# Performance work log

Measured on AMD Instinct MI355X. Metric: run time of the kernel, lower is better.

Reference implementation:

```python
import jax, jax.numpy as jnp
import numpy as np

B, N, H = 8, 2048, 1024
FF = 4 * H
EPS = 1e-5

def layer_norm(x, g, b):
    mu = jnp.mean(x, axis=-1, keepdims=True)
    var = jnp.mean(jnp.square(x - mu), axis=-1, keepdims=True)
    return (x - mu) * jax.lax.rsqrt(var + EPS) * g + b

def setup_inputs() -> dict:
    key = jax.random.key(0)
    ks = jax.random.split(key, 6)
    s1 = 1.0 / np.sqrt(H)
    s2 = 1.0 / np.sqrt(FF)
    return {
        "x": jax.random.normal(ks[0], (B, N, H), dtype=jnp.float32),
        "ln1_g": jnp.ones((H,), jnp.float32),
        "ln1_b": jnp.zeros((H,), jnp.float32),
        "ln2_g": jnp.ones((H,), jnp.float32),
        "ln2_b": jnp.zeros((H,), jnp.float32),
        "w1": jax.random.uniform(ks[1], (H, FF), jnp.float32, -s1, s1),
        "b1": jax.random.uniform(ks[2], (FF,), jnp.float32, -s1, s1),
        "w2": jax.random.uniform(ks[3], (FF, H), jnp.float32, -s2, s2),
        "b2": jax.random.uniform(ks[4], (H,), jnp.float32, -s2, s2),
    }

def reference(x, ln1_g, ln1_b, ln2_g, ln2_b, w1, b1, w2, b2):
    # raw unscaled self-attention: softmax(x x^T) x  (dropout = identity, eval mode)
    scores = jnp.einsum('bnh,bmh->bnm', x, x)          # [B,N,N]
    attn = jax.nn.softmax(scores, axis=-1)
    attended = jnp.einsum('bnm,bmh->bnh', attn, x)     # [B,N,H]
    h = layer_norm(x + attended, ln1_g, ln1_b)
    ffn = jnp.einsum('bnf,fh->bnh', jax.nn.gelu(jnp.einsum('bnh,hf->bnf', h, w1) + b1, approximate=False), w2) + b2
    return layer_norm(h + ffn, ln2_g, ln2_b)
```

## Files before the change

### kernel.cpp

```cpp
#include <hip/hip_runtime.h>
#include <stdint.h>

#define NB 8
#define NN 2048
#define HH 1024
#define FFD 4096
#define M2 8
constexpr float EPS_ = 1e-5f;

typedef _Float16 f16;
typedef _Float16 f16x8 __attribute__((ext_vector_type(8)));
typedef float f32x4 __attribute__((ext_vector_type(4)));
typedef float f32x16 __attribute__((ext_vector_type(16)));

__device__ __forceinline__ f32x4 MFMA16(f16x8 a, f16x8 b, f32x4 c) {
  return __builtin_amdgcn_mfma_f32_16x16x32_f16(a, b, c, 0, 0, 0);
}
__device__ __forceinline__ f32x16 MFMA32(f16x8 a, f16x8 b, f32x16 c) {
  return __builtin_amdgcn_mfma_f32_32x32x16_f16(a, b, c, 0, 0, 0);
}
__device__ __forceinline__ ushort h2u(f16 h) { union { f16 h; ushort u; } v; v.h = h; return v.u; }
__device__ __forceinline__ unsigned pack2(float a, float b) {
  return (unsigned)h2u((f16)a) | ((unsigned)h2u((f16)b) << 16);
}
__device__ __forceinline__ float4 ld4(const float* p) { return *(const float4*)p; }
__device__ __forceinline__ float gelu(float u) {
  return 0.5f * u * (1.0f + erff(u * 0.70710678118654752f));
}
__device__ __forceinline__ void gload16(const void* g, void* l) {
  __builtin_amdgcn_global_load_lds(
      (const __attribute__((address_space(1))) unsigned int*)g,
      (__attribute__((address_space(3))) unsigned int*)l, 16, 0, 0);
}

__global__ void convert_hl(const float* __restrict__ x, f16* __restrict__ xh,
                           f16* __restrict__ xl) {
  const size_t i = ((size_t)blockIdx.x * blockDim.x + threadIdx.x) * 4;
  float4 v = ld4(x + i);
  f16 h0 = (f16)v.x, h1 = (f16)v.y, h2 = (f16)v.z, h3 = (f16)v.w;
  ushort4 ho = {h2u(h0), h2u(h1), h2u(h2), h2u(h3)};
  ushort4 lo = {h2u((f16)(v.x - (float)h0)), h2u((f16)(v.y - (float)h1)),
                h2u((f16)(v.z - (float)h2)), h2u((f16)(v.w - (float)h3))};
  *(ushort4*)(xh + i) = ho;
  *(ushort4*)(xl + i) = lo;
}

__global__ void transpose_f16k(const float* __restrict__ src, f16* __restrict__ dst,
                               int R, int C, long sbs, long dbs) {
  __shared__ float tl[32][33];
  src += (size_t)blockIdx.z * sbs;
  dst += (size_t)blockIdx.z * dbs;
  const int t = threadIdx.x;
  const int c0 = blockIdx.x * 32, r0 = blockIdx.y * 32;
  {
    const int r = t >> 3, c4 = t & 7;
    float4 v = ld4(src + (size_t)(r0 + r) * C + c0 + c4 * 4);
    tl[r][c4 * 4 + 0] = v.x; tl[r][c4 * 4 + 1] = v.y;
    tl[r][c4 * 4 + 2] = v.z; tl[r][c4 * 4 + 3] = v.w;
  }
  __syncthreads();
  {
    const int c = t >> 3, r4 = t & 7;
    ushort4 o;
    o.x = h2u((f16)tl[r4 * 4 + 0][c]);
    o.y = h2u((f16)tl[r4 * 4 + 1][c]);
    o.z = h2u((f16)tl[r4 * 4 + 2][c]);
    o.w = h2u((f16)tl[r4 * 4 + 3][c]);
    *(ushort4*)(dst + (size_t)(c0 + c) * R + r0 + r4 * 4) = o;
  }
}

#define RSTR 528
__device__ __forceinline__ void stageKB(char* REGb, const f16* xhb, const f16* xlb,
                                        int j0, int k0, int w, int l) {
#pragma unroll
  for (int r = 0; r < 2; ++r) {
    const int grp = r * 8 + w;
    const int j = grp * 16 + (l >> 2);
    const int clog = (l & 3) ^ ((j >> 1) & 3);
    const size_t src = (size_t)(j0 + j) * HH + k0 + clog * 8;
    gload16(xhb + src, REGb + grp * 1024);
    gload16(xlb + src, REGb + 16384 + grp * 1024);
  }
}
__device__ __forceinline__ void stageVB(char* VBb, const f16* xtb, int jabs, int w, int l) {
#pragma unroll
  for (int r = 0; r < 4; ++r) {
    const int grp = r * 8 + w;
    const int h = grp * 32 + (l >> 1);
    const int clog = (l & 1) ^ ((h >> 2) & 1);
    gload16(xtb + (size_t)h * NN + jabs + clog * 8, VBb + grp * 1024);
  }
}

__global__ __launch_bounds__(512, 2)
void attn_v2(const float* __restrict__ x, const f16* __restrict__ xh,
             const f16* __restrict__ xl, const f16* __restrict__ xt,
             const float* __restrict__ g1, const float* __restrict__ lb1,
             float* __restrict__ hout) {
  extern __shared__ char smem[];
  char* REG = smem;
  char* PB  = smem + 65536;
  float* RD   = (float*)(smem + 99328);
  float* mrow = (float*)(smem + 100352);
  float* lrow = (float*)(smem + 100608);
  float* fctb = (float*)(smem + 100864);

  const int t = threadIdx.x, l = t & 63, w = t >> 6;
  const int l31 = l & 31, lh = l >> 5;
  const int wr = w >> 2, wc = w & 3;
  const int b = blockIdx.y, m0 = blockIdx.x * 64;
  const f16* __restrict__ xhb = xh + (size_t)b * NN * HH;
  const f16* __restrict__ xlb = xl + (size_t)b * NN * HH;
  const f16* __restrict__ xtb = xt + (size_t)b * HH * NN;
  const float* __restrict__ xb = x + (size_t)b * NN * HH;

  if (t < 64) { mrow[t] = -INFINITY; lrow[t] = 0.f; }

  f32x16 Oacc[8] = {};
  const int arow = m0 + wr * 32 + l31;

  for (int jt = 0; jt < 8; ++jt) {
    const int j0 = jt * 256;
    f32x16 sacc[2] = {};

    f16x8 ah[2], al[2];
#pragma unroll
    for (int s = 0; s < 2; ++s) {
      ah[s] = *(const f16x8*)(xhb + (size_t)arow * HH + s * 16 + lh * 8);
      al[s] = *(const f16x8*)(xlb + (size_t)arow * HH + s * 16 + lh * 8);
    }
    stageKB(REG, xhb, xlb, j0, 0, w, l);
    __syncthreads();
    int buf = 0;
    for (int kc = 0; kc < 32; ++kc) {
      f16x8 nh[2], nl[2];
      if (kc < 31) {
        stageKB(REG + (buf ^ 1) * 32768, xhb, xlb, j0, (kc + 1) * 32, w, l);
        const int kn = (kc + 1) * 32;
#pragma unroll
        for (int s = 0; s < 2; ++s) {
          nh[s] = *(const f16x8*)(xhb + (size_t)arow * HH + kn + s * 16 + lh * 8);
          nl[s] = *(const f16x8*)(xlb + (size_t)arow * HH + kn + s * 16 + lh * 8);
        }
      }
      const char* KH = REG + buf * 32768;
      const char* KL = KH + 16384;
#pragma unroll
      for (int ct = 0; ct < 2; ++ct) {
        const int j = wc * 64 + ct * 32 + l31;
        const int swz = (j >> 1) & 3;
        const char* rowH = KH + j * 64;
        const char* rowL = KL + j * 64;
#pragma unroll
        for (int s = 0; s < 2; ++s) {
          const int cp = (s * 2 + lh) ^ swz;
          f16x8 bh = *(const f16x8*)(rowH + cp * 16);
          f16x8 bl = *(const f16x8*)(rowL + cp * 16);
          sacc[ct] = MFMA32(ah[s], bh, sacc[ct]);
          sacc[ct] = MFMA32(al[s], bh, sacc[ct]);
          sacc[ct] = MFMA32(ah[s], bl, sacc[ct]);
        }
      }
      __syncthreads();
      if (kc < 31) {
#pragma unroll
        for (int s = 0; s < 2; ++s) { ah[s] = nh[s]; al[s] = nl[s]; }
      }
      buf ^= 1;
    }

    float tmax[16];
#pragma unroll
    for (int rg = 0; rg < 16; ++rg) tmax[rg] = fmaxf(sacc[0][rg], sacc[1][rg]);
#pragma unroll
    for (int off = 1; off <= 16; off <<= 1)
#pragma unroll
      for (int rg = 0; rg < 16; ++rg) tmax[rg] = fmaxf(tmax[rg], __shfl_xor(tmax[rg], off, 64));
    if (l31 == 0) {
#pragma unroll
      for (int rg = 0; rg < 16; ++rg) {
        const int rl = (rg & 3) + 8 * (rg >> 2) + 4 * lh;
        RD[wc * 64 + wr * 32 + rl] = tmax[rg];
      }
    }
    __syncthreads();
    if (t < 64) {
      float mt = fmaxf(fmaxf(RD[t], RD[64 + t]), fmaxf(RD[128 + t], RD[192 + t]));
      float mo = mrow[t];
      float mn = fmaxf(mo, mt);
      mrow[t] = mn;
      fctb[t] = __expf(mo - mn);
    }
    __syncthreads();
    float mv[16], psum[16];
#pragma unroll
    for (int rg = 0; rg < 16; ++rg)
      mv[rg] = mrow[wr * 32 + (rg & 3) + 8 * (rg >> 2) + 4 * lh];
#pragma unroll
    for (int ct = 0; ct < 2; ++ct) {
#pragma unroll
      for (int rg = 0; rg < 16; ++rg) {
        float p = __expf(sacc[ct][rg] - mv[rg]);
        if (ct == 0) psum[rg] = p; else psum[rg] += p;
        float po = __shfl_xor(p, 1, 64);
        if (!(l & 1)) {
          const int R = wr * 32 + (rg & 3) + 8 * (rg >> 2) + 4 * lh;
          const int col = wc * 64 + ct * 32 + l31;
          *(unsigned*)(PB + R * RSTR + col * 2) = pack2(p, po);
        }
      }
    }
#pragma unroll
    for (int off = 1; off <= 16; off <<= 1)
#pragma unroll
      for (int rg = 0; rg < 16; ++rg) psum[rg] += __shfl_xor(psum[rg], off, 64);
    if (l31 == 0) {
#pragma unroll
      for (int rg = 0; rg < 16; ++rg) {
        const int rl = (rg & 3) + 8 * (rg >> 2) + 4 * lh;
        RD[wc * 64 + wr * 32 + rl] = psum[rg];
      }
    }
    __syncthreads();
    if (t < 64) lrow[t] = lrow[t] * fctb[t] + (RD[t] + RD[64 + t] + RD[128 + t] + RD[192 + t]);
    float fv[16];
#pragma unroll
    for (int rg = 0; rg < 16; ++rg)
      fv[rg] = fctb[wr * 32 + (rg & 3) + 8 * (rg >> 2) + 4 * lh];
#pragma unroll
    for (int ht = 0; ht < 8; ++ht)
#pragma unroll
      for (int rg = 0; rg < 16; ++rg) Oacc[ht][rg] *= fv[rg];

    stageVB(REG, xtb, j0, w, l);
    __syncthreads();
    int vbuf = 0;
    for (int jc = 0; jc < 16; ++jc) {
      if (jc < 15) stageVB(REG + (vbuf ^ 1) * 32768, xtb, j0 + (jc + 1) * 16, w, l);
      const char* VBc = REG + vbuf * 32768;
      f16x8 pa = *(const f16x8*)(PB + (wr * 32 + l31) * RSTR + (jc * 2 + lh) * 16);
#pragma unroll
      for (int ht = 0; ht < 8; ++ht) {
        const int h = wc * 256 + ht * 32 + l31;
        f16x8 vb = *(const f16x8*)(VBc + h * 32 + ((lh ^ ((h >> 2) & 1)) * 16));
        Oacc[ht] = MFMA32(pa, vb, Oacc[ht]);
      }
      __syncthreads();
      vbuf ^= 1;
    }
  }

  float lv[16];
#pragma unroll
  for (int rg = 0; rg < 16; ++rg)
    lv[rg] = 1.0f / lrow[wr * 32 + (rg & 3) + 8 * (rg >> 2) + 4 * lh];
  float musum[16];
#pragma unroll
  for (int rg = 0; rg < 16; ++rg) musum[rg] = 0.f;
#pragma unroll
  for (int ht = 0; ht < 8; ++ht) {
    const int col = wc * 256 + ht * 32 + l31;
#pragma unroll
    for (int rg = 0; rg < 16; ++rg) {
      const int R = wr * 32 + (rg & 3) + 8 * (rg >> 2) + 4 * lh;
      float v = fmaf(Oacc[ht][rg], lv[rg], xb[(size_t)(m0 + R) * HH + col]);
      Oacc[ht][rg] = v; musum[rg] += v;
    }
  }
#pragma unroll
  for (int off = 1; off <= 16; off <<= 1)
#pragma unroll
    for (int rg = 0; rg < 16; ++rg) musum[rg] += __shfl_xor(musum[rg], off, 64);
  if (l31 == 0) {
#pragma unroll
    for (int rg = 0; rg < 16; ++rg) {
      const int rl = (rg & 3) + 8 * (rg >> 2) + 4 * lh;
      RD[wc * 64 + wr * 32 + rl] = musum[rg];
    }
  }
  __syncthreads();
  if (t < 64) mrow[t] = (RD[t] + RD[64 + t] + RD[128 + t] + RD[192 + t]) * (1.0f / HH);
  __syncthreads();
  float mu[16], vsum[16];
#pragma unroll
  for (int rg = 0; rg < 16; ++rg) {
    mu[rg] = mrow[wr * 32 + (rg & 3) + 8 * (rg >> 2) + 4 * lh];
    vsum[rg] = 0.f;
  }
#pragma unroll
  for (int ht = 0; ht < 8; ++ht)
#pragma unroll
    for (int rg = 0; rg < 16; ++rg) {
      float d = Oacc[ht][rg] - mu[rg];
      vsum[rg] += d * d;
    }
#pragma unroll
  for (int off = 1; off <= 16; off <<= 1)
#pragma unroll
    for (int rg = 0; rg < 16; ++rg) vsum[rg] += __shfl_xor(vsum[rg], off, 64);
  if (l31 == 0) {
#pragma unroll
    for (int rg = 0; rg < 16; ++rg) {
      const int rl = (rg & 3) + 8 * (rg >> 2) + 4 * lh;
      RD[wc * 64 + wr * 32 + rl] = vsum[rg];
    }
  }
  __syncthreads();
  if (t < 64) fctb[t] = rsqrtf((RD[t] + RD[64 + t] + RD[128 + t] + RD[192 + t]) * (1.0f / HH) + EPS_);
  __syncthreads();
  float rs[16];
#pragma unroll
  for (int rg = 0; rg < 16; ++rg)
    rs[rg] = fctb[wr * 32 + (rg & 3) + 8 * (rg >> 2) + 4 * lh];
#pragma unroll
  for (int ht = 0; ht < 8; ++ht) {
    const int col = wc * 256 + ht * 32 + l31;
    const float gv = g1[col], bv = lb1[col];
#pragma unroll
    for (int rg = 0; rg < 16; ++rg) {
      const int R = wr * 32 + (rg & 3) + 8 * (rg >> 2) + 4 * lh;
      hout[((size_t)b * NN + m0 + R) * HH + col] = (Oacc[ht][rg] - mu[rg]) * rs[rg] * gv + bv;
    }
  }
}

__global__ __launch_bounds__(1024)
void attn_legacy(const float* __restrict__ x, const float* __restrict__ g1,
                 const float* __restrict__ lb1, float* __restrict__ hout) {
  extern __shared__ char smem[];
  char* AB = smem;
  char* BB = smem + 5120;
  char* PB2 = smem + 46080;
  char* VB = smem + 62976;
  float* RD  = (float*)(smem + 144896);
  float* RD2 = (float*)(smem + 145920);

  const int t = threadIdx.x, l = t & 63, w = t >> 6;
  const int lg = l >> 4, li = l & 15;
  const int wr = w >> 3, wc = w & 7;
  const int b = blockIdx.y, m0 = blockIdx.x * 32;
  const float* __restrict__ xb = x + (size_t)b * NN * HH;

  const int ar = t >> 5, ak = t & 31;
  const int bj = t >> 2, bq = t & 3;
  const int vjp = t & 15, vhg = t >> 4;

  f32x4 Oacc[8] = {};
  float m_run[4] = {-INFINITY, -INFINITY, -INFINITY, -INFINITY};
  float l_run[4] = {0.f, 0.f, 0.f, 0.f};

  for (int jt = 0; jt < 8; ++jt) {
    const int j0 = jt * 256;
    f32x4 sacc[2] = {};
    float qv = xb[(size_t)(m0 + ar) * HH + ak];
    float4 ca = ld4(xb + (size_t)(j0 + bj) * HH + bq * 8);
    float4 cb = ld4(xb + (size_t)(j0 + bj) * HH + bq * 8 + 4);
    for (int kc = 0; kc < 32; ++kc) {
      __syncthreads();
      {
        f16 qh = (f16)qv; f16 ql = (f16)(qv - (float)qh);
        *(ushort*)(AB + ar * 80 + ak * 2) = h2u(qh);
        *(ushort*)(AB + 2560 + ar * 80 + ak * 2) = h2u(ql);
        float vv[8] = {ca.x, ca.y, ca.z, ca.w, cb.x, cb.y, cb.z, cb.w};
        f16x8 hi8, lo8;
#pragma unroll
        for (int i = 0; i < 8; ++i) {
          f16 h = (f16)vv[i]; hi8[i] = h; lo8[i] = (f16)(vv[i] - (float)h);
        }
        *(f16x8*)(BB + bj * 80 + bq * 16) = hi8;
        *(f16x8*)(BB + 20480 + bj * 80 + bq * 16) = lo8;
      }
      if (kc < 31) {
        const int k0 = (kc + 1) * 32;
        qv = xb[(size_t)(m0 + ar) * HH + k0 + ak];
        ca = ld4(xb + (size_t)(j0 + bj) * HH + k0 + bq * 8);
        cb = ld4(xb + (size_t)(j0 + bj) * HH + k0 + bq * 8 + 4);
      }
      __syncthreads();
      const int arow = wr * 16 + li;
      f16x8 ahi = *(const f16x8*)(AB + arow * 80 + lg * 16);
      f16x8 alo = *(const f16x8*)(AB + 2560 + arow * 80 + lg * 16);
#pragma unroll
      for (int ct = 0; ct < 2; ++ct) {
        const int j = wc * 32 + ct * 16 + li;
        f16x8 bhi = *(const f16x8*)(BB + j * 80 + lg * 16);
        f16x8 blo = *(const f16x8*)(BB + 20480 + j * 80 + lg * 16);
        sacc[ct] = MFMA16(ahi, bhi, sacc[ct]);
        sacc[ct] = MFMA16(ahi, blo, sacc[ct]);
        sacc[ct] = MFMA16(alo, bhi, sacc[ct]);
      }
    }
    float m[4];
#pragma unroll
    for (int r = 0; r < 4; ++r) m[r] = fmaxf(sacc[0][r], sacc[1][r]);
#pragma unroll
    for (int off = 1; off <= 8; off <<= 1)
#pragma unroll
      for (int r = 0; r < 4; ++r) m[r] = fmaxf(m[r], __shfl_xor(m[r], off, 64));
    if (li == 0)
#pragma unroll
      for (int r = 0; r < 4; ++r) RD[wc * 32 + wr * 16 + lg * 4 + r] = m[r];
    __syncthreads();
    float mnew[4], fct[4];
#pragma unroll
    for (int r = 0; r < 4; ++r) {
      const int row = wr * 16 + lg * 4 + r;
      float mt = RD[row];
#pragma unroll
      for (int w2 = 1; w2 < 8; ++w2) mt = fmaxf(mt, RD[w2 * 32 + row]);
      mnew[r] = fmaxf(m_run[r], mt);
      fct[r] = __expf(m_run[r] - mnew[r]);
      m_run[r] = mnew[r];
    }
    float psum[4] = {0.f, 0.f, 0.f, 0.f};
#pragma unroll
    for (int ct = 0; ct < 2; ++ct)
#pragma unroll
      for (int r = 0; r < 4; ++r) {
        float p = __expf(sacc[ct][r] - mnew[r]);
        psum[r] += p;
        float po = __shfl_xor(p, 1, 64);
        if (!(l & 1)) {
          const int row = wr * 16 + lg * 4 + r;
          *(unsigned*)(PB2 + row * 528 + (wc * 32 + ct * 16 + (li & 14)) * 2) = pack2(p, po);
        }
      }
#pragma unroll
    for (int off = 1; off <= 8; off <<= 1)
#pragma unroll
      for (int r = 0; r < 4; ++r) psum[r] += __shfl_xor(psum[r], off, 64);
    if (li == 0)
#pragma unroll
      for (int r = 0; r < 4; ++r) RD2[wc * 32 + wr * 16 + lg * 4 + r] = psum[r];
    __syncthreads();
#pragma unroll
    for (int r = 0; r < 4; ++r) {
      const int row = wr * 16 + lg * 4 + r;
      float ts = 0.f;
#pragma unroll
      for (int w2 = 0; w2 < 8; ++w2) ts += RD2[w2 * 32 + row];
      l_run[r] = l_run[r] * fct[r] + ts;
    }
#pragma unroll
    for (int ti = 0; ti < 8; ++ti)
#pragma unroll
      for (int r = 0; r < 4; ++r) Oacc[ti][r] *= fct[r];

    float4 v0[4], v1[4];
#pragma unroll
    for (int q = 0; q < 4; ++q) {
      v0[q] = ld4(xb + (size_t)(j0 + 2 * vjp) * HH + vhg * 16 + q * 4);
      v1[q] = ld4(xb + (size_t)(j0 + 2 * vjp + 1) * HH + vhg * 16 + q * 4);
    }
    for (int jc = 0; jc < 8; ++jc) {
      __syncthreads();
#pragma unroll
      for (int q = 0; q < 4; ++q) {
        float a0[4] = {v0[q].x, v0[q].y, v0[q].z, v0[q].w};
        float a1[4] = {v1[q].x, v1[q].y, v1[q].z, v1[q].w};
#pragma unroll
        for (int i = 0; i < 4; ++i) {
          const int h = vhg * 16 + q * 4 + i;
          *(unsigned*)(VB + h * 80 + vjp * 4) = pack2(a0[i], a1[i]);
        }
      }
      if (jc < 7) {
        const int jj = j0 + (jc + 1) * 32;
#pragma unroll
        for (int q = 0; q < 4; ++q) {
          v0[q] = ld4(xb + (size_t)(jj + 2 * vjp) * HH + vhg * 16 + q * 4);
          v1[q] = ld4(xb + (size_t)(jj + 2 * vjp + 1) * HH + vhg * 16 + q * 4);
        }
      }
      __syncthreads();
      f16x8 pa = *(const f16x8*)(PB2 + (wr * 16 + li) * 528 + jc * 64 + lg * 16);
#pragma unroll
      for (int ti = 0; ti < 8; ++ti) {
        const int h = wc * 128 + ti * 16 + li;
        f16x8 vb = *(const f16x8*)(VB + h * 80 + lg * 16);
        Oacc[ti] = MFMA16(pa, vb, Oacc[ti]);
      }
    }
  }

  float musum[4] = {0.f, 0.f, 0.f, 0.f};
#pragma unroll
  for (int ti = 0; ti < 8; ++ti) {
    const int col = wc * 128 + ti * 16 + li;
#pragma unroll
    for (int r = 0; r < 4; ++r) {
      const int row = m0 + wr * 16 + lg * 4 + r;
      float v = xb[(size_t)row * HH + col] + Oacc[ti][r] / l_run[r];
      Oacc[ti][r] = v; musum[r] += v;
    }
  }
#pragma unroll
  for (int off = 1; off <= 8; off <<= 1)
#pragma unroll
    for (int r = 0; r < 4; ++r) musum[r] += __shfl_xor(musum[r], off, 64);
  if (li == 0)
#pragma unroll
    for (int r = 0; r < 4; ++r) RD[wc * 32 + wr * 16 + lg * 4 + r] = musum[r];
  __syncthreads();
  float mu[4];
#pragma unroll
  for (int r = 0; r < 4; ++r) {
    const int row = wr * 16 + lg * 4 + r;
    float s = 0.f;
#pragma unroll
    for (int w2 = 0; w2 < 8; ++w2) s += RD[w2 * 32 + row];
    mu[r] = s * (1.0f / HH);
  }
  float vsum[4] = {0.f, 0.f, 0.f, 0.f};
#pragma unroll
  for (int ti = 0; ti < 8; ++ti)
#pragma unroll
    for (int r = 0; r < 4; ++r) {
      float d = Oacc[ti][r] - mu[r]; vsum[r] += d * d;
    }
#pragma unroll
  for (int off = 1; off <= 8; off <<= 1)
#pragma unroll
    for (int r = 0; r < 4; ++r) vsum[r] += __shfl_xor(vsum[r], off, 64);
  if (li == 0)
#pragma unroll
    for (int r = 0; r < 4; ++r) RD2[wc * 32 + wr * 16 + lg * 4 + r] = vsum[r];
  __syncthreads();
  float rs[4];
#pragma unroll
  for (int r = 0; r < 4; ++r) {
    const int row = wr * 16 + lg * 4 + r;
    float s = 0.f;
#pragma unroll
    for (int w2 = 0; w2 < 8; ++w2) s += RD2[w2 * 32 + row];
    rs[r] = rsqrtf(s * (1.0f / HH) + EPS_);
  }
#pragma unroll
  for (int ti = 0; ti < 8; ++ti) {
    const int col = wc * 128 + ti * 16 + li;
    const float gv = g1[col], bv = lb1[col];
#pragma unroll
    for (int r = 0; r < 4; ++r) {
      const int row = m0 + wr * 16 + lg * 4 + r;
      hout[((size_t)b * NN + row) * HH + col] = (Oacc[ti][r] - mu[r]) * rs[r] * gv + bv;
    }
  }
}

template<bool WS>
__global__ __launch_bounds__(1024)
void ffn_kernel(float* __restrict__ hio, const float* __restrict__ g2,
                const float* __restrict__ lb2,
                const float* __restrict__ w1, const float* __restrict__ b1f,
                const float* __restrict__ w2, const float* __restrict__ b2f,
                const f16* __restrict__ w1t, const f16* __restrict__ w2t) {
  extern __shared__ char smem[];
  char* HB  = smem;
  char* W1B = smem + 5120;
  char* GB  = smem + 25600;
  char* W2B = smem + 59392;
  float* RD  = (float*)(smem + 141312);
  float* RD2 = (float*)(smem + 142336);

  const int t = threadIdx.x, l = t & 63;
  const int w = t >> 6;
  const int lg = l >> 4, li = l & 15;
  const int rt = w >> 2, wc4 = w & 3;
  const int b = blockIdx.y, m0 = blockIdx.x * 64;
  float* __restrict__ hb = hio + ((size_t)b * NN + m0) * HH;

  f32x4 Oacc[16] = {};

  for (int ft = 0; ft < 16; ++ft) {
    const int f0 = ft * 256;
    f32x4 uacc[4] = {};
    const int hr = t >> 4, hk2 = t & 15;
    float2 hv = *(const float2*)(hb + (size_t)hr * HH + hk2 * 2);
    f16x8 wv; float4 wf0, wf1;
    const int wfW = t >> 2, wkq = t & 3;
    const int ki = t & 31, fg = t >> 5;
    if (WS) {
      wv = *(const f16x8*)(w1t + (size_t)(f0 + wfW) * HH + wkq * 8);
    } else {
      wf0 = ld4(w1 + (size_t)ki * FFD + f0 + fg * 8);
      wf1 = ld4(w1 + (size_t)ki * FFD + f0 + fg * 8 + 4);
    }
    for (int kc = 0; kc < 32; ++kc) {
      __syncthreads();
      *(unsigned*)(HB + hr * 80 + hk2 * 4) = pack2(hv.x, hv.y);
      if (WS) {
        *(f16x8*)(W1B + wfW * 80 + wkq * 16) = wv;
      } else {
        float vv[8] = {wf0.x, wf0.y, wf0.z, wf0.w, wf1.x, wf1.y, wf1.z, wf1.w};
#pragma unroll
        for (int i = 0; i < 8; ++i)
          *(ushort*)(W1B + (fg * 8 + i) * 80 + ki * 2) = h2u((f16)vv[i]);
      }
      if (kc < 31) {
        const int k0 = (kc + 1) * 32;
        hv = *(const float2*)(hb + (size_t)hr * HH + k0 + hk2 * 2);
        if (WS) wv = *(const f16x8*)(w1t + (size_t)(f0 + wfW) * HH + k0 + wkq * 8);
        else {
          wf0 = ld4(w1 + (size_t)(k0 + ki) * FFD + f0 + fg * 8);
          wf1 = ld4(w1 + (size_t)(k0 + ki) * FFD + f0 + fg * 8 + 4);
        }
      }
      __syncthreads();
      f16x8 af = *(const f16x8*)(HB + (rt * 16 + li) * 80 + lg * 16);
#pragma unroll
      for (int ct = 0; ct < 4; ++ct) {
        const int fc = wc4 * 64 + ct * 16 + li;
        f16x8 bf = *(const f16x8*)(W1B + fc * 80 + lg * 16);
        uacc[ct] = MFMA16(af, bf, uacc[ct]);
      }
    }
    __syncthreads();
    {
      const float4 b1v = *(const float4*)(b1f + f0 + 4 * t);
      (void)b1v;
    }
#pragma unroll
    for (int ct = 0; ct < 4; ++ct) {
      const int ucol = wc4 * 64 + ct * 16 + li;
      const float b1v = b1f[f0 + ucol];
#pragma unroll
      for (int r = 0; r < 4; ++r) {
        float g = gelu(uacc[ct][r] + b1v);
        float go = __shfl_xor(g, 1, 64);
        if (!(l & 1)) {
          const int row = rt * 16 + lg * 4 + r;
          *(unsigned*)(GB + row * 528 + (wc4 * 64 + ct * 16 + (li & 14)) * 2) = pack2(g, go);
        }
      }
    }
    __syncthreads();
    f16x8 wv2[4]; float4 fv[8];
    const int w2fi = t & 31, w2hg = t >> 5;
    if (WS) {
#pragma unroll
      for (int q = 0; q < 4; ++q)
        wv2[q] = *(const f16x8*)(w2t + (size_t)t * FFD + f0 + q * 8);
    } else {
#pragma unroll
      for (int q = 0; q < 8; ++q)
        fv[q] = ld4(w2 + (size_t)(f0 + w2fi) * HH + w2hg * 32 + q * 4);
    }
    for (int fc = 0; fc < 8; ++fc) {
      if (WS) {
#pragma unroll
        for (int q = 0; q < 4; ++q) *(f16x8*)(W2B + t * 80 + q * 16) = wv2[q];
      } else {
#pragma unroll
        for (int q = 0; q < 8; ++q) {
          float vv[4] = {fv[q].x, fv[q].y, fv[q].z, fv[q].w};
#pragma unroll
          for (int i = 0; i < 4; ++i)
            *(ushort*)(W2B + (w2hg * 32 + q * 4 + i) * 80 + w2fi * 2) = h2u((f16)vv[i]);
        }
      }
      if (fc < 7) {
        const int fk = f0 + (fc + 1) * 32;
        if (WS) {
#pragma unroll
          for (int q = 0; q < 4; ++q)
            wv2[q] = *(const f16x8*)(w2t + (size_t)t * FFD + fk + q * 8);
        } else {
#pragma unroll
          for (int q = 0; q < 8; ++q)
            fv[q] = ld4(w2 + (size_t)(fk + w2fi) * HH + w2hg * 32 + q * 4);
        }
      }
      __syncthreads();
      f16x8 ag = *(const f16x8*)(GB + (rt * 16 + li) * 528 + fc * 64 + lg * 16);
#pragma unroll
      for (int ti = 0; ti < 16; ++ti) {
        const int h = wc4 * 256 + ti * 16 + li;
        f16x8 bg = *(const f16x8*)(W2B + h * 80 + lg * 16);
        Oacc[ti] = MFMA16(ag, bg, Oacc[ti]);
      }
      __syncthreads();
    }
  }

  const float4 dummy = {0,0,0,0}; (void)dummy;
  float musum[4] = {0.f, 0.f, 0.f, 0.f};
#pragma unroll
  for (int ti = 0; ti < 16; ++ti) {
    const int col = wc4 * 256 + ti * 16 + li;
    const float b2v = b2f[col];
#pragma unroll
    for (int r = 0; r < 4; ++r) {
      const int row = rt * 16 + lg * 4 + r;
      float v = hb[(size_t)row * HH + col] + Oacc[ti][r] + b2v;
      Oacc[ti][r] = v; musum[r] += v;
    }
  }
#pragma unroll
  for (int off = 1; off <= 8; off <<= 1)
#pragma unroll
    for (int r = 0; r < 4; ++r) musum[r] += __shfl_xor(musum[r], off, 64);
  if (li == 0)
#pragma unroll
    for (int r = 0; r < 4; ++r) RD[wc4 * 64 + rt * 16 + lg * 4 + r] = musum[r];
  __syncthreads();
  float mu[4];
#pragma unroll
  for (int r = 0; r < 4; ++r) {
    const int row = rt * 16 + lg * 4 + r;
    float s = 0.f;
#pragma unroll
    for (int w2i = 0; w2i < 4; ++w2i) s += RD[w2i * 64 + row];
    mu[r] = s * (1.0f / HH);
  }
  float vsum[4] = {0.f, 0.f, 0.f, 0.f};
#pragma unroll
  for (int ti = 0; ti < 16; ++ti)
#pragma unroll
    for (int r = 0; r < 4; ++r) { float d = Oacc[ti][r] - mu[r]; vsum[r] += d * d; }
#pragma unroll
  for (int off = 1; off <= 8; off <<= 1)
#pragma unroll
    for (int r = 0; r < 4; ++r) vsum[r] += __shfl_xor(vsum[r], off, 64);
  if (li == 0)
#pragma unroll
    for (int r = 0; r < 4; ++r) RD2[wc4 * 64 + rt * 16 + lg * 4 + r] = vsum[r];
  __syncthreads();
  float rs[4];
#pragma unroll
  for (int r = 0; r < 4; ++r) {
    const int row = rt * 16 + lg * 4 + r;
    float s = 0.f;
#pragma unroll
    for (int w2i = 0; w2i < 4; ++w2i) s += RD2[w2i * 64 + row];
    rs[r] = rsqrtf(s * (1.0f / HH) + EPS_);
  }
#pragma unroll
  for (int ti = 0; ti < 16; ++ti) {
    const int col = wc4 * 256 + ti * 16 + li;
    const float gv = g2[col], bv = lb2[col];
#pragma unroll
    for (int r = 0; r < 4; ++r) {
      const int row = rt * 16 + lg * 4 + r;
      hb[(size_t)row * HH + col] = (Oacc[ti][r] - mu[r]) * rs[r] * gv + bv;
    }
  }
}

extern "C" void kernel_launch(void* const* d_in, const int* in_sizes, int n_in,
                              void* d_out, int out_size, void* d_ws, size_t ws_size,
                              hipStream_t stream) {
  (void)in_sizes; (void)n_in; (void)out_size;
  const float* x    = (const float*)d_in[0];
  const float* ln1g = (const float*)d_in[1];
  const float* ln1b = (const float*)d_in[2];
  const float* ln2g = (const float*)d_in[3];
  const float* ln2b = (const float*)d_in[4];
  const float* w1   = (const float*)d_in[5];
  const float* bb1  = (const float*)d_in[6];
  const float* w2   = (const float*)d_in[7];
  const float* bb2  = (const float*)d_in[8];
  float* out = (float*)d_out;

  const size_t wN   = (size_t)FFD * HH;
  const size_t xN   = (size_t)NB * NN * HH;
  const size_t need_w    = 2 * wN * sizeof(f16);
  const size_t need_full = need_w + 3 * xN * sizeof(f16);
  const bool ws_w    = (ws_size >= need_w) && d_ws;
  const bool ws_full = (ws_size >= need_full) && d_ws;

  f16* w1t = (f16*)d_ws;
  f16* w2t = w1t + wN;
  f16* xh  = w2t + wN;
  f16* xl  = xh + xN;
  f16* xt  = xl + xN;

  (void)hipFuncSetAttribute((const void*)attn_v2,
                            hipFuncAttributeMaxDynamicSharedMemorySize, 101376);
  (void)hipFuncSetAttribute((const void*)attn_legacy,
                            hipFuncAttributeMaxDynamicSharedMemorySize, 146944);
  (void)hipFuncSetAttribute((const void*)ffn_kernel<true>,
                            hipFuncAttributeMaxDynamicSharedMemorySize, 143360);
  (void)hipFuncSetAttribute((const void*)ffn_kernel<false>,
                            hipFuncAttributeMaxDynamicSharedMemorySize, 143360);

  if (ws_w) {
    transpose_f16k<<<dim3(FFD / 32, HH / 32, 1), 256, 0, stream>>>(w1, w1t, HH, FFD, 0, 0);
    transpose_f16k<<<dim3(HH / 32, FFD / 32, 1), 256, 0, stream>>>(w2, w2t, FFD, HH, 0, 0);
  }
  if (ws_full) {
    convert_hl<<<(int)(xN / 4 / 256), 256, 0, stream>>>(x, xh, xl);
    transpose_f16k<<<dim3(HH / 32, NN / 32, NB), 256, 0, stream>>>(
        x, xt, NN, HH, (long)NN * HH, (long)HH * NN);
    attn_v2<<<dim3(NN / 64, NB), 512, 101376, stream>>>(x, xh, xl, xt, ln1g, ln1b, out);
  } else {
    attn_legacy<<<dim3(NN / 32, NB), 1024, 146944, stream>>>(x, ln1g, ln1b, out);
  }
  if (ws_w)
    ffn_kernel<true><<<dim3(NN / 64, NB), 1024, 143360, stream>>>(
        out, ln2g, ln2b, w1, bb1, w2, bb2, w1t, w2t);
  else
    ffn_kernel<false><<<dim3(NN / 64, NB), 1024, 143360, stream>>>(
        out, ln2g, ln2b, w1, bb1, w2, bb2, nullptr, nullptr);
}
```

Baseline: 1.666 ms.

## Add FFN kernel with async-LDS double-buffered weights and 32x32 MFMA

Adds ffn_v2, which streams pre-transposed f16 W1/W2 tiles into swizzled, double-buffered LDS with global_load_lds and computes both GEMMs with 32x32x16 MFMAs. The attention kernel can now also write an f16 copy of its LayerNorm output, so the FFN reads half-width activations directly. The aim is to overlap weight staging with compute, cut LDS traffic and the per-chunk conversion overhead, and use less LDS per block. In exchange it needs extra workspace for the f16 copy and adds an extra global write in the attention kernel.

```diff
diff --git a/kernel.cpp b/kernel.cpp
--- a/kernel.cpp
+++ b/kernel.cpp
@@ -5,7 +5,6 @@
 #define NN 2048
 #define HH 1024
 #define FFD 4096
-#define M2 8
 constexpr float EPS_ = 1e-5f;
 
 typedef _Float16 f16;
@@ -31,6 +30,13 @@
   __builtin_amdgcn_global_load_lds(
       (const __attribute__((address_space(1))) unsigned int*)g,
       (__attribute__((address_space(3))) unsigned int*)l, 16, 0, 0);
+}
+__device__ __forceinline__ f16x8 cvt8(const float* p) {
+  float4 a = ld4(p), b = ld4(p + 4);
+  union { unsigned u[4]; f16x8 v; } cv;
+  cv.u[0] = pack2(a.x, a.y); cv.u[1] = pack2(a.z, a.w);
+  cv.u[2] = pack2(b.x, b.y); cv.u[3] = pack2(b.z, b.w);
+  return cv.v;
 }
 
 __global__ void convert_hl(const float* __restrict__ x, f16* __restrict__ xh,
@@ -93,11 +99,12 @@
   }
 }
 
+template<bool WH>
 __global__ __launch_bounds__(512, 2)
 void attn_v2(const float* __restrict__ x, const f16* __restrict__ xh,
              const f16* __restrict__ xl, const f16* __restrict__ xt,
              const float* __restrict__ g1, const float* __restrict__ lb1,
-             float* __restrict__ hout) {
+             float* __restrict__ hout, f16* __restrict__ h16) {
   extern __shared__ char smem[];
   char* REG = smem;
   char* PB  = smem + 65536;
@@ -320,7 +327,212 @@
 #pragma unroll
     for (int rg = 0; rg < 16; ++rg) {
       const int R = wr * 32 + (rg & 3) + 8 * (rg >> 2) + 4 * lh;
-      hout[((size_t)b * NN + m0 + R) * HH + col] = (Oacc[ht][rg] - mu[rg]) * rs[rg] * gv + bv;
+      const float ov = (Oacc[ht][rg] - mu[rg]) * rs[rg] * gv + bv;
+      hout[((size_t)b * NN + m0 + R) * HH + col] = ov;
+      if (WH) h16[((size_t)b * NN + m0 + R) * HH + col] = (f16)ov;
+    }
+  }
+}
+
+__device__ __forceinline__ void stageW1(char* dst, const f16* w1t, int f0, int k0,
+                                        int w, int l) {
+#pragma unroll
+  for (int r = 0; r < 2; ++r) {
+    const int grp = r * 16 + w;
+    const int row = grp * 8 + (l >> 3);
+    const int sl = (l & 7) ^ (row & 7);
+    gload16(w1t + (size_t)(f0 + row) * HH + k0 + sl * 8, dst + grp * 1024);
+  }
+}
+__device__ __forceinline__ void stageW2(char* dst, const f16* w2t, int fabs,
+                                        int w, int l) {
+#pragma unroll
+  for (int r = 0; r < 2; ++r) {
+    const int grp = r * 16 + w;
+    const int h = grp * 32 + (l >> 1);
+    const int clog = (l & 1) ^ ((h >> 2) & 1);
+    gload16(w2t + (size_t)h * FFD + fabs + clog * 8, dst + grp * 1024);
+  }
+}
+
+template<bool HF>
+__global__ __launch_bounds__(1024)
+void ffn_v2(float* __restrict__ hio, const f16* __restrict__ h16,
+            const float* __restrict__ g2, const float* __restrict__ lb2,
+            const float* __restrict__ b1f, const float* __restrict__ b2f,
+            const f16* __restrict__ w1t, const f16* __restrict__ w2t) {
+  extern __shared__ char smem[];
+  char* REG = smem;
+  char* GB  = smem + 65536;
+  float* RD  = (float*)(smem + 98304);
+  float* MUB = (float*)(smem + 100352);
+  float* RSB = (float*)(smem + 100608);
+
+  const int t = threadIdx.x, l = t & 63, w = t >> 6;
+  const int l31 = l & 31, lh = l >> 5;
+  const int wr = w >> 3, wc = w & 7;
+  const int b = blockIdx.y, m0 = blockIdx.x * 64;
+  float* __restrict__ hb = hio + ((size_t)b * NN + m0) * HH;
+  const f16* __restrict__ h16b = HF ? (h16 + ((size_t)b * NN + m0) * HH) : nullptr;
+
+  const int myrow = wr * 32 + l31;
+  f32x16 Oacc[4] = {};
+
+  for (int ft = 0; ft < 16; ++ft) {
+    const int f0 = ft * 256;
+    f32x16 sacc = {};
+
+    stageW1(REG, w1t, f0, 0, w, l);
+    f16x8 ah[4];
+#pragma unroll
+    for (int s = 0; s < 4; ++s) {
+      if (HF) ah[s] = *(const f16x8*)(h16b + (size_t)myrow * HH + s * 16 + lh * 8);
+      else    ah[s] = cvt8(hb + (size_t)myrow * HH + s * 16 + lh * 8);
+    }
+    __syncthreads();
+    int buf = 0;
+    for (int kc = 0; kc < 16; ++kc) {
+      f16x8 na[4];
+      if (kc < 15) {
+        const int kn = (kc + 1) * 64;
+        stageW1(REG + (buf ^ 1) * 32768, w1t, f0, kn, w, l);
+#pragma unroll
+        for (int s = 0; s < 4; ++s) {
+          if (HF) na[s] = *(const f16x8*)(h16b + (size_t)myrow * HH + kn + s * 16 + lh * 8);
+          else    na[s] = cvt8(hb + (size_t)myrow * HH + kn + s * 16 + lh * 8);
+        }
+      }
+      const char* W = REG + buf * 32768;
+      const int j = wc * 32 + l31;
+      const char* rb = W + j * 128;
+      const int key = j & 7;
+#pragma unroll
+      for (int s = 0; s < 4; ++s) {
+        const int p = (s * 2 + lh) ^ key;
+        f16x8 bf = *(const f16x8*)(rb + p * 16);
+        sacc = MFMA32(ah[s], bf, sacc);
+      }
+      __syncthreads();
+      if (kc < 15) {
+#pragma unroll
+        for (int s = 0; s < 4; ++s) ah[s] = na[s];
+      }
+      buf ^= 1;
+    }
+
+    {
+      const int fcol = wc * 32 + l31;
+      const float b1v = b1f[f0 + fcol];
+#pragma unroll
+      for (int rg = 0; rg < 16; ++rg) {
+        float g = gelu(sacc[rg] + b1v);
+        float go = __shfl_xor(g, 1, 64);
+        if (!(l & 1)) {
+          const int row = wr * 32 + (rg & 3) + 8 * (rg >> 2) + 4 * lh;
+          const int s = fcol >> 3;
+          const int p = s ^ (row & 31);
+          *(unsigned*)(GB + row * 512 + p * 16 + (fcol & 7) * 2) = pack2(g, go);
+        }
+      }
+    }
+    __syncthreads();
+
+    stageW2(REG, w2t, f0, w, l);
+    __syncthreads();
+    int vb_ = 0;
+    for (int fc = 0; fc < 16; ++fc) {
+      if (fc < 15) stageW2(REG + (vb_ ^ 1) * 32768, w2t, f0 + (fc + 1) * 16, w, l);
+      const char* Vc = REG + vb_ * 32768;
+      const int ps = (fc * 2 + lh) ^ (myrow & 31);
+      f16x8 pa = *(const f16x8*)(GB + myrow * 512 + ps * 16);
+#pragma unroll
+      for (int ht = 0; ht < 4; ++ht) {
+        const int h = wc * 128 + ht * 32 + l31;
+        f16x8 vb = *(const f16x8*)(Vc + h * 32 + ((lh ^ ((h >> 2) & 1)) * 16));
+        Oacc[ht] = MFMA32(pa, vb, Oacc[ht]);
+      }
+      __syncthreads();
+      vb_ ^= 1;
+    }
+  }
+
+  float musum[16];
+#pragma unroll
+  for (int rg = 0; rg < 16; ++rg) musum[rg] = 0.f;
+#pragma unroll
+  for (int ht = 0; ht < 4; ++ht) {
+    const int col = wc * 128 + ht * 32 + l31;
+    const float b2v = b2f[col];
+#pragma unroll
+    for (int rg = 0; rg < 16; ++rg) {
+      const int row = wr * 32 + (rg & 3) + 8 * (rg >> 2) + 4 * lh;
+      float v = hb[(size_t)row * HH + col] + Oacc[ht][rg] + b2v;
+      Oacc[ht][rg] = v; musum[rg] += v;
+    }
+  }
+#pragma unroll
+  for (int off = 1; off <= 16; off <<= 1)
+#pragma unroll
+    for (int rg = 0; rg < 16; ++rg) musum[rg] += __shfl_xor(musum[rg], off, 64);
+  if (l31 == 0) {
+#pragma unroll
+    for (int rg = 0; rg < 16; ++rg) {
+      const int rl = (rg & 3) + 8 * (rg >> 2) + 4 * lh;
+      RD[wc * 64 + wr * 32 + rl] = musum[rg];
+    }
+  }
+  __syncthreads();
+  if (t < 64) {
+    float s = 0.f;
+#pragma unroll
+    for (int q = 0; q < 8; ++q) s += RD[q * 64 + t];
+    MUB[t] = s * (1.0f / HH);
+  }
+  __syncthreads();
+  float mu[16], vsum[16];
+#pragma unroll
+  for (int rg = 0; rg < 16; ++rg) {
+    mu[rg] = MUB[wr * 32 + (rg & 3) + 8 * (rg >> 2) + 4 * lh];
+    vsum[rg] = 0.f;
+  }
+#pragma unroll
+  for (int ht = 0; ht < 4; ++ht)
+#pragma unroll
+    for (int rg = 0; rg < 16; ++rg) {
+      float d = Oacc[ht][rg] - mu[rg];
+      vsum[rg] += d * d;
+    }
+#pragma unroll
+  for (int off = 1; off <= 16; off <<= 1)
+#pragma unroll
+    for (int rg = 0; rg < 16; ++rg) vsum[rg] += __shfl_xor(vsum[rg], off, 64);
+  if (l31 == 0) {
+#pragma unroll
+    for (int rg = 0; rg < 16; ++rg) {
+      const int rl = (rg & 3) + 8 * (rg >> 2) + 4 * lh;
+      RD[wc * 64 + wr * 32 + rl] = vsum[rg];
+    }
+  }
+  __syncthreads();
+  if (t < 64) {
+    float s = 0.f;
+#pragma unroll
+    for (int q = 0; q < 8; ++q) s += RD[q * 64 + t];
+    RSB[t] = rsqrtf(s * (1.0f / HH) + EPS_);
+  }
+  __syncthreads();
+  float rs[16];
+#pragma unroll
+  for (int rg = 0; rg < 16; ++rg)
+    rs[rg] = RSB[wr * 32 + (rg & 3) + 8 * (rg >> 2) + 4 * lh];
+#pragma unroll
+  for (int ht = 0; ht < 4; ++ht) {
+    const int col = wc * 128 + ht * 32 + l31;
+    const float gv = g2[col], bv = lb2[col];
+#pragma unroll
+    for (int rg = 0; rg < 16; ++rg) {
+      const int row = wr * 32 + (rg & 3) + 8 * (rg >> 2) + 4 * lh;
+      hb[(size_t)row * HH + col] = (Oacc[ht][rg] - mu[rg]) * rs[rg] * gv + bv;
     }
   }
 }
@@ -548,13 +760,11 @@
   }
 }
 
-template<bool WS>
 __global__ __launch_bounds__(1024)
-void ffn_kernel(float* __restrict__ hio, const float* __restrict__ g2,
+void ffn_legacy(float* __restrict__ hio, const float* __restrict__ g2,
                 const float* __restrict__ lb2,
                 const float* __restrict__ w1, const float* __restrict__ b1f,
-                const float* __restrict__ w2, const float* __restrict__ b2f,
-                const f16* __restrict__ w1t, const f16* __restrict__ w2t) {
+                const float* __restrict__ w2, const float* __restrict__ b2f) {
   extern __shared__ char smem[];
   char* HB  = smem;
   char* W1B = smem + 5120;
@@ -577,21 +787,14 @@
     f32x4 uacc[4] = {};
     const int hr = t >> 4, hk2 = t & 15;
     float2 hv = *(const float2*)(hb + (size_t)hr * HH + hk2 * 2);
-    f16x8 wv; float4 wf0, wf1;
-    const int wfW = t >> 2, wkq = t & 3;
+    float4 wf0, wf1;
     const int ki = t & 31, fg = t >> 5;
-    if (WS) {
-      wv = *(const f16x8*)(w1t + (size_t)(f0 + wfW) * HH + wkq * 8);
-    } else {
-      wf0 = ld4(w1 + (size_t)ki * FFD + f0 + fg * 8);
-      wf1 = ld4(w1 + (size_t)ki * FFD + f0 + fg * 8 + 4);
-    }
+    wf0 = ld4(w1 + (size_t)ki * FFD + f0 + fg * 8);
+    wf1 = ld4(w1 + (size_t)ki * FFD + f0 + fg * 8 + 4);
     for (int kc = 0; kc < 32; ++kc) {
       __syncthreads();
       *(unsigned*)(HB + hr * 80 + hk2 * 4) = pack2(hv.x, hv.y);
-      if (WS) {
-        *(f16x8*)(W1B + wfW * 80 + wkq * 16) = wv;
-      } else {
+      {
         float vv[8] = {wf0.x, wf0.y, wf0.z, wf0.w, wf1.x, wf1.y, wf1.z, wf1.w};
 #pragma unroll
         for (int i = 0; i < 8; ++i)
@@ -600,11 +803,8 @@
       if (kc < 31) {
         const int k0 = (kc + 1) * 32;
         hv = *(const float2*)(hb + (size_t)hr * HH + k0 + hk2 * 2);
-        if (WS) wv = *(const f16x8*)(w1t + (size_t)(f0 + wfW) * HH + k0 + wkq * 8);
-        else {
-          wf0 = ld4(w1 + (size_t)(k0 + ki) * FFD + f0 + fg * 8);
-          wf1 = ld4(w1 + (size_t)(k0 + ki) * FFD + f0 + fg * 8 + 4);
-        }
+        wf0 = ld4(w1 + (size_t)(k0 + ki) * FFD + f0 + fg * 8);
+        wf1 = ld4(w1 + (size_t)(k0 + ki) * FFD + f0 + fg * 8 + 4);
       }
       __syncthreads();
       f16x8 af = *(const f16x8*)(HB + (rt * 16 + li) * 80 + lg * 16);
@@ -616,10 +816,6 @@
       }
     }
     __syncthreads();
-    {
-      const float4 b1v = *(const float4*)(b1f + f0 + 4 * t);
-      (void)b1v;
-    }
 #pragma unroll
     for (int ct = 0; ct < 4; ++ct) {
       const int ucol = wc4 * 64 + ct * 16 + li;
@@ -635,41 +831,24 @@
       }
     }
     __syncthreads();
-    f16x8 wv2[4]; float4 fv[8];
+    float4 fv[8];
     const int w2fi = t & 31, w2hg = t >> 5;
-    if (WS) {
-#pragma unroll
-      for (int q = 0; q < 4; ++q)
-        wv2[q] = *(const f16x8*)(w2t + (size_t)t * FFD + f0 + q * 8);
-    } else {
-#pragma unroll
-      for (int q = 0; q < 8; ++q)
-        fv[q] = ld4(w2 + (size_t)(f0 + w2fi) * HH + w2hg * 32 + q * 4);
-    }
+#pragma unroll
+    for (int q = 0; q < 8; ++q)
+      fv[q] = ld4(w2 + (size_t)(f0 + w2fi) * HH + w2hg * 32 + q * 4);
     for (int fc = 0; fc < 8; ++fc) {
-      if (WS) {
-#pragma unroll
-        for (int q = 0; q < 4; ++q) *(f16x8*)(W2B + t * 80 + q * 16) = wv2[q];
-      } else {
-#pragma unroll
-        for (int q = 0; q < 8; ++q) {
-          float vv[4] = {fv[q].x, fv[q].y, fv[q].z, fv[q].w};
-#pragma unroll
-          for (int i = 0; i < 4; ++i)
-            *(ushort*)(W2B + (w2hg * 32 + q * 4 + i) * 80 + w2fi * 2) = h2u((f16)vv[i]);
-        }
+#pragma unroll
+      for (int q = 0; q < 8; ++q) {
+        float vv[4] = {fv[q].x, fv[q].y, fv[q].z, fv[q].w};
+#pragma unroll
+        for (int i = 0; i < 4; ++i)
+          *(ushort*)(W2B + (w2hg * 32 + q * 4 + i) * 80 + w2fi * 2) = h2u((f16)vv[i]);
       }
       if (fc < 7) {
         const int fk = f0 + (fc + 1) * 32;
-        if (WS) {
-#pragma unroll
-          for (int q = 0; q < 4; ++q)
-            wv2[q] = *(const f16x8*)(w2t + (size_t)t * FFD + fk + q * 8);
-        } else {
-#pragma unroll
-          for (int q = 0; q < 8; ++q)
-            fv[q] = ld4(w2 + (size_t)(fk + w2fi) * HH + w2hg * 32 + q * 4);
-        }
+#pragma unroll
+        for (int q = 0; q < 8; ++q)
+          fv[q] = ld4(w2 + (size_t)(fk + w2fi) * HH + w2hg * 32 + q * 4);
       }
       __syncthreads();
       f16x8 ag = *(const f16x8*)(GB + (rt * 16 + li) * 528 + fc * 64 + lg * 16);
@@ -683,7 +862,6 @@
     }
   }
 
-  const float4 dummy = {0,0,0,0}; (void)dummy;
   float musum[4] = {0.f, 0.f, 0.f, 0.f};
 #pragma unroll
   for (int ti = 0; ti < 16; ++ti) {
@@ -762,44 +940,61 @@
   const float* bb2  = (const float*)d_in[8];
   float* out = (float*)d_out;
 
-  const size_t wN   = (size_t)FFD * HH;
-  const size_t xN   = (size_t)NB * NN * HH;
+  const size_t wN = (size_t)FFD * HH;
+  const size_t xN = (size_t)NB * NN * HH;
   const size_t need_w    = 2 * wN * sizeof(f16);
-  const size_t need_full = need_w + 3 * xN * sizeof(f16);
+  const size_t need_attn = need_w + 3 * xN * sizeof(f16);
+  const size_t need_h16  = need_attn + xN * sizeof(f16);
   const bool ws_w    = (ws_size >= need_w) && d_ws;
-  const bool ws_full = (ws_size >= need_full) && d_ws;
+  const bool ws_attn = (ws_size >= need_attn) && d_ws;
+  const bool ws_h16  = (ws_size >= need_h16) && d_ws;
 
   f16* w1t = (f16*)d_ws;
   f16* w2t = w1t + wN;
   f16* xh  = w2t + wN;
   f16* xl  = xh + xN;
   f16* xt  = xl + xN;
-
-  (void)hipFuncSetAttribute((const void*)attn_v2,
+  f16* h16 = xt + xN;
+
+  (void)hipFuncSetAttribute((const void*)attn_v2<true>,
+                            hipFuncAttributeMaxDynamicSharedMemorySize, 101376);
+  (void)hipFuncSetAttribute((const void*)attn_v2<false>,
                             hipFuncAttributeMaxDynamicSharedMemorySize, 101376);
   (void)hipFuncSetAttribute((const void*)attn_legacy,
                             hipFuncAttributeMaxDynamicSharedMemorySize, 146944);
-  (void)hipFuncSetAttribute((const void*)ffn_kernel<true>,
-                            hipFuncAttributeMaxDynamicSharedMemorySize, 143360);
-  (void)hipFuncSetAttribute((const void*)ffn_kernel<false>,
+  (void)hipFuncSetAttribute((const void*)ffn_v2<true>,
+                            hipFuncAttributeMaxDynamicSharedMemorySize, 100864);
+  (void)hipFuncSetAttribute((const void*)ffn_v2<false>,
+                            hipFuncAttributeMaxDynamicSharedMemorySize, 100864);
+  (void)hipFuncSetAttribute((const void*)ffn_legacy,
                             hipFuncAttributeMaxDynamicSharedMemorySize, 143360);
 
   if (ws_w) {
     transpose_f16k<<<dim3(FFD / 32, HH / 32, 1), 256, 0, stream>>>(w1, w1t, HH, FFD, 0, 0);
     transpose_f16k<<<dim3(HH / 32, FFD / 32, 1), 256, 0, stream>>>(w2, w2t, FFD, HH, 0, 0);
   }
-  if (ws_full) {
+  if (ws_attn) {
     convert_hl<<<(int)(xN / 4 / 256), 256, 0, stream>>>(x, xh, xl);
     transpose_f16k<<<dim3(HH / 32, NN / 32, NB), 256, 0, stream>>>(
         x, xt, NN, HH, (long)NN * HH, (long)HH * NN);
-    attn_v2<<<dim3(NN / 64, NB), 512, 101376, stream>>>(x, xh, xl, xt, ln1g, ln1b, out);
+    if (ws_h16)
+      attn_v2<true><<<dim3(NN / 64, NB), 512, 101376, stream>>>(
+          x, xh, xl, xt, ln1g, ln1b, out, h16);
+    else
+      attn_v2<false><<<dim3(NN / 64, NB), 512, 101376, stream>>>(
+          x, xh, xl, xt, ln1g, ln1b, out, nullptr);
   } else {
     attn_legacy<<<dim3(NN / 32, NB), 1024, 146944, stream>>>(x, ln1g, ln1b, out);
   }
-  if (ws_w)
-    ffn_kernel<true><<<dim3(NN / 64, NB), 1024, 143360, stream>>>(
-        out, ln2g, ln2b, w1, bb1, w2, bb2, w1t, w2t);
-  else
-    ffn_kernel<false><<<dim3(NN / 64, NB), 1024, 143360, stream>>>(
-        out, ln2g, ln2b, w1, bb1, w2, bb2, nullptr, nullptr);
-}
+  if (ws_w) {
+    if (ws_h16)
+      ffn_v2<true><<<dim3(NN / 64, NB), 1024, 100864, stream>>>(
+          out, h16, ln2g, ln2b, bb1, bb2, w1t, w2t);
+    else
+      ffn_v2<false><<<dim3(NN / 64, NB), 1024, 100864, stream>>>(
+          out, nullptr, ln2g, ln2b, bb1, bb2, w1t, w2t);
+  } else {
+    ffn_legacy<<<dim3(NN / 64, NB), 1024, 143360, stream>>>(
+        out, ln2g, ln2b, w1, bb1, w2, bb2);
+  }
+}
```

Result: slower. 2.313 ms (+38.8%).
